# Kernel optimization log

Hardware: AMD Instinct MI355X
Metric: run time of the kernel (lower is better)

Reference implementation:

```python
import jax, jax.numpy as jnp
import numpy as np

DIM = 256
HEADS = 8
DIM_HEAD = 32
B, M, N = 2, 4096, 32
EPS = 1e-5


def layernorm(x, w, b):
    mu = jnp.mean(x, axis=-1, keepdims=True)
    var = jnp.mean(jnp.square(x - mu), axis=-1, keepdims=True)
    return (x - mu) * jax.lax.rsqrt(var + EPS) * w + b


def setup_inputs() -> dict:
    key = jax.random.key(0)
    ks = jax.random.split(key, 16)
    HD = HEADS * DIM_HEAD
    s = 0.02
    return {
        "x": jax.random.normal(ks[0], (B, M, DIM), jnp.float32),
        "y": jax.random.normal(ks[1], (B, M, N, DIM), jnp.float32),
        "lnq_w": jnp.ones((DIM,), jnp.float32), "lnq_b": jnp.zeros((DIM,), jnp.float32),
        "Wq": jax.random.normal(ks[2], (HD, DIM), jnp.float32) * s,
        "bq": jnp.zeros((HD,), jnp.float32),
        "lnk_w": jnp.ones((DIM,), jnp.float32), "lnk_b": jnp.zeros((DIM,), jnp.float32),
        "Wk": jax.random.normal(ks[3], (HD, DIM), jnp.float32) * s,
        "bk": jnp.zeros((HD,), jnp.float32),
        "lnv_w": jnp.ones((DIM,), jnp.float32), "lnv_b": jnp.zeros((DIM,), jnp.float32),
        "Wv": jax.random.normal(ks[4], (HD, DIM), jnp.float32) * s,
        "bv": jnp.zeros((HD,), jnp.float32),
        "Wp": jax.random.normal(ks[5], (DIM, HD), jnp.float32) * s,
        "bp": jnp.zeros((DIM,), jnp.float32),
        "pre_w": jnp.ones((DIM,), jnp.float32), "pre_b": jnp.zeros((DIM,), jnp.float32),
        "W1": jax.random.normal(ks[6], (2 * DIM, DIM), jnp.float32) * s,
        "b1": jnp.zeros((2 * DIM,), jnp.float32),
        "W2": jax.random.normal(ks[7], (DIM, 2 * DIM), jnp.float32) * s,
        "b2": jnp.zeros((DIM,), jnp.float32),
        "post_w": jnp.ones((DIM,), jnp.float32), "post_b": jnp.zeros((DIM,), jnp.float32),
    }


def reference(x, y, lnq_w, lnq_b, Wq, bq, lnk_w, lnk_b, Wk, bk,
              lnv_w, lnv_b, Wv, bv, Wp, bp, pre_w, pre_b,
              W1, b1, W2, b2, post_w, post_b):
    scale = DIM_HEAD ** -0.5
    # projections (norm then linear)
    q = layernorm(x, lnq_w, lnq_b) @ Wq.T + bq          # (B,M,H*D)
    k = layernorm(y, lnk_w, lnk_b) @ Wk.T + bk          # (B,M,N,H*D)
    v = layernorm(y, lnv_w, lnv_b) @ Wv.T + bv          # (B,M,N,H*D)
    q = q.reshape(B, M, HEADS, DIM_HEAD)
    k = k.reshape(B, M, N, HEADS, DIM_HEAD)
    v = v.reshape(B, M, N, HEADS, DIM_HEAD)
    # per-node attention: each (b,m,h) query attends over its N neighbors
    logits = scale * jnp.einsum('bmhd,bmnhd->bmnh', q, k)   # (B,M,N,H)
    attn = jax.nn.softmax(logits, axis=2)                    # softmax over N
    a = jnp.einsum('bmnh,bmnhd->bmhd', attn, v)              # (B,M,H,D)
    a = a.reshape(B, M, HEADS * DIM_HEAD)
    z = a @ Wp.T + bp
    z = layernorm(z, pre_w, pre_b)
    h = jax.nn.gelu(z @ W1.T + b1, approximate=False) @ W2.T + b2
    z = z + h
    z = layernorm(z, post_w, post_b)
    return z
```

## Files before the change

### kernel.cpp

```cpp
#include <hip/hip_runtime.h>

#define LNEPS 1e-5f

typedef short bf16x8 __attribute__((ext_vector_type(8)));
typedef float f32x4 __attribute__((ext_vector_type(4)));

#define WQ_OFF    0
#define WKT_OFF   65536
#define WV_OFF    131072
#define WPHI_OFF  196608
#define W1_OFF    262144
#define W2_OFF    393216
#define WPLO_OFF  524288
#define BVA_OFF   589824
#define T_OFF     590336
#define AG_OFF    17367552

__device__ __forceinline__ unsigned short f2bf(float f) {
    union { float f; unsigned int u; } a; a.f = f;
    unsigned int u = a.u;
    unsigned int r = (u + 0x7fffu + ((u >> 16) & 1u)) >> 16;
    return (unsigned short)r;
}
__device__ __forceinline__ float bf2f(unsigned short h) {
    union { unsigned int u; float f; } a; a.u = ((unsigned int)h) << 16;
    return a.f;
}

__device__ __forceinline__ void rowstats(float4 v, float& mu, float& inv) {
    float s  = v.x + v.y + v.z + v.w;
    float ss = v.x * v.x + v.y * v.y + v.z * v.z + v.w * v.w;
    #pragma unroll
    for (int off = 32; off; off >>= 1) {
        s  += __shfl_xor(s, off);
        ss += __shfl_xor(ss, off);
    }
    mu  = s * (1.f / 256.f);
    float var = ss * (1.f / 256.f) - mu * mu;
    inv = rsqrtf(fmaxf(var, 0.f) + LNEPS);
}

__global__ void prep_weights(const float* __restrict__ Wq, const float* __restrict__ Wk,
                             const float* __restrict__ Wv, const float* __restrict__ Wp,
                             const float* __restrict__ W1, const float* __restrict__ W2,
                             const float* __restrict__ lnk_w, const float* __restrict__ lnv_w,
                             unsigned short* __restrict__ ws) {
    int i = blockIdx.x * 256 + threadIdx.x;
    if (i < 65536)       { ws[i] = f2bf(Wq[i]); }
    else if (i < 131072) { int l = i - 65536; int dp = l >> 8, o = l & 255;
                           ws[i] = f2bf(Wk[o * 256 + dp] * lnk_w[dp]); }
    else if (i < 196608) { int l = i - 131072; int dp = l & 255;
                           ws[i] = f2bf(Wv[l] * lnv_w[dp]); }
    else if (i < 262144) { ws[i] = f2bf(Wp[i - 196608]); }
    else if (i < 393216) { ws[i] = f2bf(W1[i - 262144]); }
    else if (i < 524288) { ws[i] = f2bf(W2[i - 393216]); }
    else if (i < 589824) { float w = Wp[i - 524288]; ws[i] = f2bf(w - bf2f(f2bf(w))); }
}

__global__ void prep_bias(const float* __restrict__ Wv, const float* __restrict__ lnv_b,
                          const float* __restrict__ bv, float* __restrict__ bva) {
    int o = threadIdx.x;
    float acc = bv[o];
    #pragma unroll 4
    for (int dp = 0; dp < 256; dp += 4) {
        float4 w = *(const float4*)(Wv + o * 256 + dp);
        float4 g = *(const float4*)(lnv_b + dp);
        acc += w.x * g.x + w.y * g.y + w.z * g.z + w.w * g.w;
    }
    bva[o] = acc;
}

__global__ __launch_bounds__(256, 2)
void qt_kernel(const float* __restrict__ x,
               const float* __restrict__ lnq_w, const float* __restrict__ lnq_b,
               const float* __restrict__ bq,
               const unsigned short* __restrict__ wsb, unsigned short* __restrict__ Tg) {
    const int tid  = threadIdx.x;
    const int lane = tid & 63;
    const int wid  = tid >> 6;
    const int q4   = lane >> 4;
    const int l16  = lane & 15;
    const int b    = blockIdx.x >> 8;
    const int m0   = (blockIdx.x & 255) * 16;
    const float scale = 0.17677669529663687f;

    const unsigned short* Wq_bf  = wsb + WQ_OFF;
    const unsigned short* WkT_bf = wsb + WKT_OFF;

    __shared__ __align__(16) unsigned short lnX[16][264];
    __shared__ __align__(16) unsigned short sQ[16][264];

    {
        const float4 w4 = *(const float4*)(lnq_w + lane * 4);
        const float4 g4 = *(const float4*)(lnq_b + lane * 4);
        float4 xv[4];
        #pragma unroll
        for (int rr = 0; rr < 4; rr++) {
            int m = wid * 4 + rr;
            xv[rr] = *(const float4*)(x + (size_t)(b * 4096 + m0 + m) * 256 + lane * 4);
        }
        #pragma unroll
        for (int rr = 0; rr < 4; rr++) {
            int m = wid * 4 + rr;
            float mu, inv; rowstats(xv[rr], mu, inv);
            float4 v = xv[rr];
            ushort4 o;
            o.x = f2bf((v.x - mu) * inv * w4.x + g4.x);
            o.y = f2bf((v.y - mu) * inv * w4.y + g4.y);
            o.z = f2bf((v.z - mu) * inv * w4.z + g4.z);
            o.w = f2bf((v.w - mu) * inv * w4.w + g4.w);
            *(ushort4*)&lnX[m][lane * 4] = o;
        }
    }
    __syncthreads();

    {
        f32x4 acc[4];
        #pragma unroll
        for (int j = 0; j < 4; j++) acc[j] = 0.f;
        #pragma unroll
        for (int k = 0; k < 8; k++) {
            bf16x8 af = *(const bf16x8*)&lnX[l16][k * 32 + q4 * 8];
            #pragma unroll
            for (int j = 0; j < 4; j++) {
                int o = wid * 64 + j * 16 + l16;
                bf16x8 bfv = *(const bf16x8*)(Wq_bf + o * 256 + k * 32 + q4 * 8);
                acc[j] = __builtin_amdgcn_mfma_f32_16x16x32_bf16(af, bfv, acc[j], 0, 0, 0);
            }
        }
        #pragma unroll
        for (int j = 0; j < 4; j++) {
            int o = wid * 64 + j * 16 + l16;
            float bqv = bq[o];
            #pragma unroll
            for (int r = 0; r < 4; r++) {
                sQ[q4 * 4 + r][o] = f2bf((acc[j][r] + bqv) * scale);
            }
        }
    }
    __syncthreads();

    {
        const size_t rowbase = (size_t)(b * 4096 + m0) * 2048;
        #pragma unroll
        for (int h = 0; h < 8; h++) {
            bf16x8 af = *(const bf16x8*)&sQ[l16][h * 32 + q4 * 8];
            #pragma unroll
            for (int t = 0; t < 4; t++) {
                const int dp0 = (wid * 4 + t) * 16;
                bf16x8 bfv = *(const bf16x8*)(WkT_bf + (size_t)(dp0 + l16) * 256 + h * 32 + q4 * 8);
                f32x4 acc = {0.f, 0.f, 0.f, 0.f};
                acc = __builtin_amdgcn_mfma_f32_16x16x32_bf16(af, bfv, acc, 0, 0, 0);
                #pragma unroll
                for (int r = 0; r < 4; r++) {
                    int ml = q4 * 4 + r;
                    Tg[rowbase + (size_t)ml * 2048 + h * 256 + dp0 + l16] = f2bf(acc[r]);
                }
            }
        }
    }
}

__global__ __launch_bounds__(256, 4)
void attn_kernel(const float* __restrict__ y,
                 const unsigned short* __restrict__ wsb,
                 float* __restrict__ ag) {
    const int tid  = threadIdx.x;
    const int lane = tid & 63;
    const int wid  = tid >> 6;
    const int r    = blockIdx.x;

    const unsigned short* Wv_bf = wsb + WV_OFF;
    const unsigned short* Tg    = wsb + T_OFF;
    const float*          bva   = (const float*)(wsb + BVA_OFF);

    __shared__ __align__(16) unsigned short Y[32][264];
    __shared__ __align__(16) float Tl[8][260];
    __shared__ __align__(16) float Usm[8][260];
    __shared__ __align__(16) float sP[32][8];

    {
        bf16x8 t8 = *(const bf16x8*)(Tg + (size_t)r * 2048 + tid * 8);
        const int h = tid >> 5, d0 = (tid & 31) * 8;
        #pragma unroll
        for (int j = 0; j < 8; j++) Tl[h][d0 + j] = bf2f((unsigned short)t8[j]);
    }
    {
        const float* yb = y + (size_t)r * 8192;
        float4 vv[8];
        #pragma unroll
        for (int u = 0; u < 8; u++) {
            int n = wid * 8 + u;
            vv[u] = *(const float4*)(yb + n * 256 + lane * 4);
        }
        #pragma unroll
        for (int u = 0; u < 8; u++) {
            int n = wid * 8 + u;
            float mu, inv; rowstats(vv[u], mu, inv);
            float4 v = vv[u];
            ushort4 o;
            o.x = f2bf((v.x - mu) * inv);
            o.y = f2bf((v.y - mu) * inv);
            o.z = f2bf((v.z - mu) * inv);
            o.w = f2bf((v.w - mu) * inv);
            *(ushort4*)&Y[n][lane * 4] = o;
        }
    }
    __syncthreads();

    {
        const int n = tid >> 3, h = tid & 7;
        float acc = 0.f;
        #pragma unroll 8
        for (int dv = 0; dv < 32; dv++) {
            bf16x8 y8 = *(const bf16x8*)&Y[n][dv * 8];
            float4 ta = *(const float4*)&Tl[h][dv * 8];
            float4 tb = *(const float4*)&Tl[h][dv * 8 + 4];
            acc += bf2f((unsigned short)y8[0]) * ta.x;
            acc += bf2f((unsigned short)y8[1]) * ta.y;
            acc += bf2f((unsigned short)y8[2]) * ta.z;
            acc += bf2f((unsigned short)y8[3]) * ta.w;
            acc += bf2f((unsigned short)y8[4]) * tb.x;
            acc += bf2f((unsigned short)y8[5]) * tb.y;
            acc += bf2f((unsigned short)y8[6]) * tb.z;
            acc += bf2f((unsigned short)y8[7]) * tb.w;
        }
        sP[n][h] = acc;
    }
    __syncthreads();

    {
        const int h = tid >> 5, n = tid & 31;
        float v = sP[n][h];
        float mx = v;
        #pragma unroll
        for (int off = 16; off; off >>= 1) mx = fmaxf(mx, __shfl_xor(mx, off));
        float e = __expf(v - mx);
        float s = e;
        #pragma unroll
        for (int off = 16; off; off >>= 1) s += __shfl_xor(s, off);
        sP[n][h] = e / s;
    }
    __syncthreads();

    {
        const int dp = tid;
        float acc[8];
        #pragma unroll
        for (int h = 0; h < 8; h++) acc[h] = 0.f;
        #pragma unroll 8
        for (int n = 0; n < 32; n++) {
            float yv = bf2f(Y[n][dp]);
            float4 pA = *(const float4*)&sP[n][0];
            float4 pB = *(const float4*)&sP[n][4];
            acc[0] += pA.x * yv; acc[1] += pA.y * yv;
            acc[2] += pA.z * yv; acc[3] += pA.w * yv;
            acc[4] += pB.x * yv; acc[5] += pB.y * yv;
            acc[6] += pB.z * yv; acc[7] += pB.w * yv;
        }
        #pragma unroll
        for (int h = 0; h < 8; h++) Usm[h][dp] = acc[h];
    }
    __syncthreads();

    {
        const int o = tid, h = o >> 5;
        float acc = 0.f;
        #pragma unroll 8
        for (int dpv = 0; dpv < 32; dpv++) {
            bf16x8 wv8 = *(const bf16x8*)(Wv_bf + (size_t)o * 256 + dpv * 8);
            float4 ua = *(const float4*)&Usm[h][dpv * 8];
            float4 ub = *(const float4*)&Usm[h][dpv * 8 + 4];
            acc += bf2f((unsigned short)wv8[0]) * ua.x;
            acc += bf2f((unsigned short)wv8[1]) * ua.y;
            acc += bf2f((unsigned short)wv8[2]) * ua.z;
            acc += bf2f((unsigned short)wv8[3]) * ua.w;
            acc += bf2f((unsigned short)wv8[4]) * ub.x;
            acc += bf2f((unsigned short)wv8[5]) * ub.y;
            acc += bf2f((unsigned short)wv8[6]) * ub.z;
            acc += bf2f((unsigned short)wv8[7]) * ub.w;
        }
        ag[(size_t)r * 256 + o] = acc + bva[o];
    }
}

__global__ __launch_bounds__(256, 2)
void tail_kernel(const float* __restrict__ ag,
                 const float* __restrict__ bp,
                 const float* __restrict__ pre_w, const float* __restrict__ pre_b,
                 const float* __restrict__ b1, const float* __restrict__ b2,
                 const float* __restrict__ post_w, const float* __restrict__ post_b,
                 const unsigned short* __restrict__ wsb,
                 float* __restrict__ out) {
    const int tid  = threadIdx.x;
    const int lane = tid & 63;
    const int wid  = tid >> 6;
    const int q4   = lane >> 4;
    const int l16  = lane & 15;
    const int b    = blockIdx.x >> 8;
    const int m0   = (blockIdx.x & 255) * 16;

    const unsigned short* Wp_bf   = wsb + WPHI_OFF;
    const unsigned short* W1_bf   = wsb + W1_OFF;
    const unsigned short* W2_bf   = wsb + W2_OFF;
    const unsigned short* Wplo_bf = wsb + WPLO_OFF;

    __shared__ __align__(16) float Z[16][260];
    __shared__ __align__(16) unsigned short G[16][520];
    __shared__ __align__(16) unsigned short sQ[16][264];
    __shared__ __align__(16) float sAf[16][260];

    #pragma unroll
    for (int rr = 0; rr < 4; rr++) {
        int m = wid * 4 + rr;
        *(float4*)&sAf[m][lane * 4] =
            *(const float4*)(ag + (size_t)(b * 4096 + m0 + m) * 256 + lane * 4);
    }
    __syncthreads();

    {
        f32x4 acc[4];
        #pragma unroll
        for (int j = 0; j < 4; j++) acc[j] = 0.f;
        #pragma unroll
        for (int k = 0; k < 8; k++) {
            float4 va = *(const float4*)&sAf[l16][k * 32 + q4 * 8];
            float4 vb = *(const float4*)&sAf[l16][k * 32 + q4 * 8 + 4];
            float vs[8] = {va.x, va.y, va.z, va.w, vb.x, vb.y, vb.z, vb.w};
            bf16x8 ah, al;
            #pragma unroll
            for (int j = 0; j < 8; j++) {
                unsigned short hi = f2bf(vs[j]);
                ah[j] = (short)hi;
                al[j] = (short)f2bf(vs[j] - bf2f(hi));
            }
            #pragma unroll
            for (int j = 0; j < 4; j++) {
                int o = wid * 64 + j * 16 + l16;
                bf16x8 bh = *(const bf16x8*)(Wp_bf   + o * 256 + k * 32 + q4 * 8);
                bf16x8 bl = *(const bf16x8*)(Wplo_bf + o * 256 + k * 32 + q4 * 8);
                acc[j] = __builtin_amdgcn_mfma_f32_16x16x32_bf16(ah, bh, acc[j], 0, 0, 0);
                acc[j] = __builtin_amdgcn_mfma_f32_16x16x32_bf16(al, bh, acc[j], 0, 0, 0);
                acc[j] = __builtin_amdgcn_mfma_f32_16x16x32_bf16(ah, bl, acc[j], 0, 0, 0);
            }
        }
        #pragma unroll
        for (int j = 0; j < 4; j++) {
            int o = wid * 64 + j * 16 + l16;
            float bpv = bp[o];
            #pragma unroll
            for (int r = 0; r < 4; r++) Z[q4 * 4 + r][o] = acc[j][r] + bpv;
        }
    }
    __syncthreads();
    {
        const float4 w4 = *(const float4*)(pre_w + lane * 4);
        const float4 g4 = *(const float4*)(pre_b + lane * 4);
        #pragma unroll
        for (int rr = 0; rr < 4; rr++) {
            int m = wid * 4 + rr;
            float4 v = *(const float4*)&Z[m][lane * 4];
            float mu, inv; rowstats(v, mu, inv);
            float4 z;
            z.x = (v.x - mu) * inv * w4.x + g4.x;
            z.y = (v.y - mu) * inv * w4.y + g4.y;
            z.z = (v.z - mu) * inv * w4.z + g4.z;
            z.w = (v.w - mu) * inv * w4.w + g4.w;
            *(float4*)&Z[m][lane * 4] = z;
            ushort4 o;
            o.x = f2bf(z.x); o.y = f2bf(z.y); o.z = f2bf(z.z); o.w = f2bf(z.w);
            *(ushort4*)&sQ[m][lane * 4] = o;
        }
    }
    __syncthreads();
    {
        f32x4 acc[8];
        #pragma unroll
        for (int j = 0; j < 8; j++) acc[j] = 0.f;
        #pragma unroll
        for (int k = 0; k < 8; k++) {
            bf16x8 af = *(const bf16x8*)&sQ[l16][k * 32 + q4 * 8];
            #pragma unroll
            for (int j = 0; j < 8; j++) {
                int f = wid * 128 + j * 16 + l16;
                bf16x8 bfv = *(const bf16x8*)(W1_bf + f * 256 + k * 32 + q4 * 8);
                acc[j] = __builtin_amdgcn_mfma_f32_16x16x32_bf16(af, bfv, acc[j], 0, 0, 0);
            }
        }
        #pragma unroll
        for (int j = 0; j < 8; j++) {
            int f = wid * 128 + j * 16 + l16;
            float b1v = b1[f];
            #pragma unroll
            for (int r = 0; r < 4; r++) {
                float vz = acc[j][r] + b1v;
                float g = 0.5f * vz * (1.f + erff(vz * 0.7071067811865475f));
                G[q4 * 4 + r][f] = f2bf(g);
            }
        }
    }
    __syncthreads();
    {
        f32x4 acc[4];
        #pragma unroll
        for (int j = 0; j < 4; j++) acc[j] = 0.f;
        #pragma unroll
        for (int k = 0; k < 16; k++) {
            bf16x8 af = *(const bf16x8*)&G[l16][k * 32 + q4 * 8];
            #pragma unroll
            for (int j = 0; j < 4; j++) {
                int o = wid * 64 + j * 16 + l16;
                bf16x8 bfv = *(const bf16x8*)(W2_bf + o * 512 + k * 32 + q4 * 8);
                acc[j] = __builtin_amdgcn_mfma_f32_16x16x32_bf16(af, bfv, acc[j], 0, 0, 0);
            }
        }
        #pragma unroll
        for (int j = 0; j < 4; j++) {
            int o = wid * 64 + j * 16 + l16;
            float b2v = b2[o];
            #pragma unroll
            for (int r = 0; r < 4; r++) Z[q4 * 4 + r][o] += acc[j][r] + b2v;
        }
    }
    __syncthreads();
    {
        const float4 w4 = *(const float4*)(post_w + lane * 4);
        const float4 g4 = *(const float4*)(post_b + lane * 4);
        #pragma unroll
        for (int rr = 0; rr < 4; rr++) {
            int m = wid * 4 + rr;
            float4 v = *(const float4*)&Z[m][lane * 4];
            float mu, inv; rowstats(v, mu, inv);
            float4 o;
            o.x = (v.x - mu) * inv * w4.x + g4.x;
            o.y = (v.y - mu) * inv * w4.y + g4.y;
            o.z = (v.z - mu) * inv * w4.z + g4.z;
            o.w = (v.w - mu) * inv * w4.w + g4.w;
            *(float4*)(out + (size_t)(b * 4096 + m0 + m) * 256 + lane * 4) = o;
        }
    }
}

extern "C" void kernel_launch(void* const* d_in, const int* in_sizes, int n_in,
                              void* d_out, int out_size, void* d_ws, size_t ws_size,
                              hipStream_t stream) {
    (void)in_sizes; (void)n_in; (void)out_size; (void)ws_size;
    const float* x      = (const float*)d_in[0];
    const float* y      = (const float*)d_in[1];
    const float* lnq_w  = (const float*)d_in[2];
    const float* lnq_b  = (const float*)d_in[3];
    const float* Wq     = (const float*)d_in[4];
    const float* bq     = (const float*)d_in[5];
    const float* lnk_w  = (const float*)d_in[6];
    const float* Wk     = (const float*)d_in[8];
    const float* lnv_w  = (const float*)d_in[10];
    const float* lnv_b  = (const float*)d_in[11];
    const float* Wv     = (const float*)d_in[12];
    const float* bv     = (const float*)d_in[13];
    const float* Wp     = (const float*)d_in[14];
    const float* bp     = (const float*)d_in[15];
    const float* pre_w  = (const float*)d_in[16];
    const float* pre_b  = (const float*)d_in[17];
    const float* W1     = (const float*)d_in[18];
    const float* b1     = (const float*)d_in[19];
    const float* W2     = (const float*)d_in[20];
    const float* b2     = (const float*)d_in[21];
    const float* post_w = (const float*)d_in[22];
    const float* post_b = (const float*)d_in[23];
    unsigned short* wsb = (unsigned short*)d_ws;
    float* bva = (float*)(wsb + BVA_OFF);
    unsigned short* Tg = wsb + T_OFF;
    float* ag = (float*)(wsb + AG_OFF);

    prep_weights<<<2304, 256, 0, stream>>>(Wq, Wk, Wv, Wp, W1, W2, lnk_w, lnv_w, wsb);
    prep_bias<<<1, 256, 0, stream>>>(Wv, lnv_b, bv, bva);
    qt_kernel<<<512, 256, 0, stream>>>(x, lnq_w, lnq_b, bq, wsb, Tg);
    attn_kernel<<<8192, 256, 0, stream>>>(y, wsb, ag);
    tail_kernel<<<512, 256, 0, stream>>>(ag, bp, pre_w, pre_b, b1, b2, post_w, post_b,
                                         wsb, (float*)d_out);
}
```

Measured before the change: 599.9 us.

## Compute V projection per neighbor with MFMA before softmax-weighted reduction

The attention kernel used to form U = P^T·Y per head with scalar FMAs, store it to shared memory, and then apply Wv with scalar dot products. Now each wave computes V = Y·Wv^T for all 32 neighbors on bf16 MFMA tiles held in registers. The softmax weights are applied afterwards, with a cross-lane shuffle reduction. This drops the Usm buffer and one barrier and moves the projection onto matrix cores. In exchange it does more FLOPs (32 rows instead of 8 head-rows) and adds accumulator register pressure.

```diff
diff --git a/kernel.cpp b/kernel.cpp
--- a/kernel.cpp
+++ b/kernel.cpp
@@ -168,6 +168,8 @@
     const int tid  = threadIdx.x;
     const int lane = tid & 63;
     const int wid  = tid >> 6;
+    const int q4   = lane >> 4;
+    const int l16  = lane & 15;
     const int r    = blockIdx.x;
 
     const unsigned short* Wv_bf = wsb + WV_OFF;
@@ -176,8 +178,7 @@
 
     __shared__ __align__(16) unsigned short Y[32][264];
     __shared__ __align__(16) float Tl[8][260];
-    __shared__ __align__(16) float Usm[8][260];
-    __shared__ __align__(16) float sP[32][8];
+    __shared__ __align__(16) float sP[32][9];
 
     {
         bf16x8 t8 = *(const bf16x8*)(Tg + (size_t)r * 2048 + tid * 8);
@@ -207,6 +208,24 @@
         }
     }
     __syncthreads();
+
+    f32x4 vacc[2][4];
+    #pragma unroll
+    for (int nt = 0; nt < 2; nt++)
+        #pragma unroll
+        for (int j = 0; j < 4; j++) vacc[nt][j] = 0.f;
+    #pragma unroll
+    for (int k = 0; k < 8; k++) {
+        bf16x8 a0 = *(const bf16x8*)&Y[l16][k * 32 + q4 * 8];
+        bf16x8 a1 = *(const bf16x8*)&Y[16 + l16][k * 32 + q4 * 8];
+        #pragma unroll
+        for (int j = 0; j < 4; j++) {
+            int o = wid * 64 + j * 16 + l16;
+            bf16x8 bv8 = *(const bf16x8*)(Wv_bf + (size_t)o * 256 + k * 32 + q4 * 8);
+            vacc[0][j] = __builtin_amdgcn_mfma_f32_16x16x32_bf16(a0, bv8, vacc[0][j], 0, 0, 0);
+            vacc[1][j] = __builtin_amdgcn_mfma_f32_16x16x32_bf16(a1, bv8, vacc[1][j], 0, 0, 0);
+        }
+    }
 
     {
         const int n = tid >> 3, h = tid & 7;
@@ -244,43 +263,32 @@
     __syncthreads();
 
     {
-        const int dp = tid;
-        float acc[8];
-        #pragma unroll
-        for (int h = 0; h < 8; h++) acc[h] = 0.f;
-        #pragma unroll 8
-        for (int n = 0; n < 32; n++) {
-            float yv = bf2f(Y[n][dp]);
-            float4 pA = *(const float4*)&sP[n][0];
-            float4 pB = *(const float4*)&sP[n][4];
-            acc[0] += pA.x * yv; acc[1] += pA.y * yv;
-            acc[2] += pA.z * yv; acc[3] += pA.w * yv;
-            acc[4] += pB.x * yv; acc[5] += pB.y * yv;
-            acc[6] += pB.z * yv; acc[7] += pB.w * yv;
-        }
-        #pragma unroll
-        for (int h = 0; h < 8; h++) Usm[h][dp] = acc[h];
-    }
-    __syncthreads();
-
-    {
-        const int o = tid, h = o >> 5;
-        float acc = 0.f;
-        #pragma unroll 8
-        for (int dpv = 0; dpv < 32; dpv++) {
-            bf16x8 wv8 = *(const bf16x8*)(Wv_bf + (size_t)o * 256 + dpv * 8);
-            float4 ua = *(const float4*)&Usm[h][dpv * 8];
-            float4 ub = *(const float4*)&Usm[h][dpv * 8 + 4];
-            acc += bf2f((unsigned short)wv8[0]) * ua.x;
-            acc += bf2f((unsigned short)wv8[1]) * ua.y;
-            acc += bf2f((unsigned short)wv8[2]) * ua.z;
-            acc += bf2f((unsigned short)wv8[3]) * ua.w;
-            acc += bf2f((unsigned short)wv8[4]) * ub.x;
-            acc += bf2f((unsigned short)wv8[5]) * ub.y;
-            acc += bf2f((unsigned short)wv8[6]) * ub.z;
-            acc += bf2f((unsigned short)wv8[7]) * ub.w;
-        }
-        ag[(size_t)r * 256 + o] = acc + bva[o];
+        const int h0 = 2 * wid, h1 = 2 * wid + 1;
+        float pa[4];
+        #pragma unroll
+        for (int j = 0; j < 4; j++) pa[j] = 0.f;
+        #pragma unroll
+        for (int idx = 0; idx < 4; idx++) {
+            const int n0 = q4 * 4 + idx, n1 = 16 + q4 * 4 + idx;
+            float p00 = sP[n0][h0], p01 = sP[n0][h1];
+            float p10 = sP[n1][h0], p11 = sP[n1][h1];
+            pa[0] += p00 * vacc[0][0][idx] + p10 * vacc[1][0][idx];
+            pa[1] += p00 * vacc[0][1][idx] + p10 * vacc[1][1][idx];
+            pa[2] += p01 * vacc[0][2][idx] + p11 * vacc[1][2][idx];
+            pa[3] += p01 * vacc[0][3][idx] + p11 * vacc[1][3][idx];
+        }
+        #pragma unroll
+        for (int j = 0; j < 4; j++) {
+            pa[j] += __shfl_xor(pa[j], 16);
+            pa[j] += __shfl_xor(pa[j], 32);
+        }
+        if (q4 == 0) {
+            #pragma unroll
+            for (int j = 0; j < 4; j++) {
+                int o = wid * 64 + j * 16 + l16;
+                ag[(size_t)r * 256 + o] = pa[j] + bva[o];
+            }
+        }
     }
 }
 
```

Result: no change. 594.6 us (-0.9%).
